# Kernel tuning notes

Hardware: AMD Instinct MI355X
Metric: run time of the kernel (lower is better)

The kernel has to match this reference:

```python
import jax, jax.numpy as jnp
import numpy as np

N_GAUSS = 1536
WIDTH, HEIGHT = 160, 128
FX = FY = 146.44        # 2343.024 * (160/2560)
CX, CY = WIDTH / 2.0, HEIGHT / 2.0
EPS2D = 0.3             # 2D covariance dilation (as in prepare_rasterization_coefficients)
NEAR, FAR = 0.01, 1e10


def eval_sh_basis(dirs):
    # real SH basis up to degree 3, 16 components (matches eval_sh_old)
    x, y, z = dirs[..., 0], dirs[..., 1], dirs[..., 2]
    one = jnp.ones_like(x)
    return jnp.stack([
        0.282095 * one,
        -0.488603 * y, 0.488603 * z, -0.488603 * x,
        1.092548 * x * y, -1.092548 * y * z, 0.315392 * (3 * z * z - 1),
        -1.092548 * x * z, 0.546274 * (x * x - y * y),
        -0.590044 * y * (3 * x * x - y * y), 2.890611 * x * y * z,
        -0.457046 * y * (5 * z * z - 1), 0.373176 * z * (5 * z * z - 3),
        -0.457046 * x * (5 * z * z - 1), 1.445306 * z * (x * x - y * y),
        -0.590044 * x * (x * x - 3 * y * y)], axis=-1)


def quat_to_rot(q):
    q = q / jnp.linalg.norm(q, axis=1, keepdims=True)
    w, x, y, z = q[:, 0], q[:, 1], q[:, 2], q[:, 3]
    R = jnp.stack([
        1 - 2 * (y * y + z * z), 2 * (x * y - z * w), 2 * (x * z + y * w),
        2 * (x * y + z * w), 1 - 2 * (x * x + z * z), 2 * (y * z - x * w),
        2 * (x * z - y * w), 2 * (y * z + x * w), 1 - 2 * (x * x + y * y)], axis=-1)
    return R.reshape(-1, 3, 3)


def get_viewmat(c2w):
    # c2w: (B,3,4); flip y/z camera axes then invert (matches torch get_viewmat)
    R = c2w[:, :3, :3] * jnp.array([[[1.0, -1.0, -1.0]]], dtype=c2w.dtype)
    t = c2w[:, :3, 3:4]
    R_inv = jnp.swapaxes(R, 1, 2)
    t_inv = -(R_inv @ t)
    return R_inv[0], t_inv[0, :, 0]


def setup_inputs() -> dict:
    key = jax.random.key(0)
    k0, k1, k2, k3, k4, k5 = jax.random.split(key, 6)
    N = N_GAUSS
    xy = jax.random.normal(k0, (N, 2), dtype=jnp.float32) * 0.5
    # world z negative -> positive camera-frame depth after axis flip
    z = -(1.0 + 4.0 * jax.random.uniform(k1, (N, 1), dtype=jnp.float32))
    means = jnp.concatenate([xy, z], axis=1)
    quats = jax.random.normal(k2, (N, 4), dtype=jnp.float32)
    log_scales = jax.random.normal(k3, (N, 3), dtype=jnp.float32) * 0.3 - 3.0
    opacity_logits = jax.random.normal(k4, (N,), dtype=jnp.float32)
    sh_coeffs = jax.random.normal(k5, (N, 16, 3), dtype=jnp.float32) * 0.3
    camera_to_worlds = jnp.eye(4, dtype=jnp.float32)[None, :3, :]
    return {"means": means, "quats": quats, "log_scales": log_scales,
            "opacity_logits": opacity_logits, "sh_coeffs": sh_coeffs,
            "camera_to_worlds": camera_to_worlds}


def reference(means, quats, log_scales, opacity_logits, sh_coeffs, camera_to_worlds):
    R_w2c, t_w2c = get_viewmat(camera_to_worlds)
    means_cam = means @ R_w2c.T + t_w2c                    # (N,3)
    depth = means_cam[:, 2]
    mask = (depth > NEAR) & (depth < FAR)

    # view-dependent colors from SH (degree 3)
    cam_pos = camera_to_worlds[0, :3, 3]
    dirs = means - cam_pos
    dirs = dirs / jnp.linalg.norm(dirs, axis=1, keepdims=True)
    colors = jnp.maximum(jnp.einsum('nk,nkc->nc', eval_sh_basis(dirs), sh_coeffs) + 0.5, 0.0)

    # 3D covariance -> camera frame -> EWA 2D projection
    Rg = quat_to_rot(quats)                                 # (N,3,3)
    M = Rg * jnp.exp(log_scales)[:, None, :]                # R @ diag(S)
    cov3d = M @ jnp.swapaxes(M, 1, 2)
    cov_cam = jnp.einsum('ij,njk,lk->nil', R_w2c, cov3d, R_w2c)
    tx, ty, tz = means_cam[:, 0], means_cam[:, 1], means_cam[:, 2]
    rz = 1.0 / tz
    zero = jnp.zeros_like(rz)
    J = jnp.stack([jnp.stack([FX * rz, zero, -FX * tx * rz * rz], -1),
                   jnp.stack([zero, FY * rz, -FY * ty * rz * rz], -1)], -2)  # (N,2,3)
    cov2d = jnp.einsum('nij,njk,nlk->nil', J, cov_cam, J)
    a = cov2d[:, 0, 0] + EPS2D
    c = cov2d[:, 1, 1] + EPS2D
    b = cov2d[:, 0, 1]
    det = a * c - b * b
    A, B, C = c / det, -b / det, a / det                    # conic (inverse 2D cov)

    u = FX * tx * rz + CX
    v = FY * ty * rz + CY
    opac = jax.nn.sigmoid(opacity_logits)

    px = jnp.arange(WIDTH, dtype=means.dtype)
    py = jnp.arange(HEIGHT, dtype=means.dtype)
    dx = px[None, None, :] - u[:, None, None]               # (N,1,W)
    dy = py[None, :, None] - v[:, None, None]               # (N,H,1)
    power = (-0.5 * (A[:, None, None] * dx * dx + C[:, None, None] * dy * dy)
             - B[:, None, None] * (dx * dy))                # (N,H,W)
    alpha = jnp.minimum(0.999, opac[:, None, None] * jnp.exp(power))
    alpha = jnp.where(mask[:, None, None], alpha, 0.0)

    # global depth sort (front-to-back alpha compositing)
    order = jnp.argsort(jnp.where(mask, depth, jnp.inf))
    alpha = alpha[order]
    colors = colors[order]
    T = jnp.cumprod(1.0 - alpha, axis=0)
    T_excl = jnp.concatenate([jnp.ones_like(T[:1]), T[:-1]], axis=0)
    w = T_excl * alpha                                      # (N,H,W)
    rgb = jnp.einsum('nhw,nc->hwc', w, colors)              # (H,W,3)
    return rgb
```

## Files before the change

### kernel.cpp

```cpp
#include <hip/hip_runtime.h>
#include <math.h>

#define N_GAUSS 1536
#define WIDTH   160
#define HEIGHT  128
#define NPIX    (WIDTH * HEIGHT)
#define FXC     146.44f
#define FYC     146.44f
#define CXC     80.0f
#define CYC     64.0f
#define EPS2D   0.3f
#define NEARP   0.01f
#define FARP    1e10f
#define CHUNK   128
#define NCHUNK  (N_GAUSS / CHUNK)
#define REC     12
#define L2E     1.4426950408889634f

#define PREP_BLOCKS 384
#define PREP_TPB    256
#define SCAN_LEN4   (N_GAUSS / 64 / 4)

__device__ __forceinline__ float fast_exp2(float x) {
    return __builtin_amdgcn_exp2f(x);
}


__global__ __launch_bounds__(PREP_TPB) void prep_sort_kernel(
    const float* __restrict__ means, const float* __restrict__ quats,
    const float* __restrict__ log_scales, const float* __restrict__ opac_logits,
    const float* __restrict__ sh, const float* __restrict__ c2w,
    float* __restrict__ sorted)
{
    __shared__ float4 k4_lds[N_GAUSS / 4];
    float* k_lds = (float*)k4_lds;

    float C[12];
#pragma unroll
    for (int k = 0; k < 12; k++) C[k] = c2w[k];
    float R00 =  C[0], R01 =  C[4], R02 =  C[8];
    float R10 = -C[1], R11 = -C[5], R12 = -C[9];
    float R20 = -C[2], R21 = -C[6], R22 = -C[10];
    float cpx = C[3], cpy = C[7], cpz = C[11];
    float t0 = -(R00 * cpx + R01 * cpy + R02 * cpz);
    float t1 = -(R10 * cpx + R11 * cpy + R12 * cpz);
    float t2 = -(R20 * cpx + R21 * cpy + R22 * cpz);

    for (int j = threadIdx.x; j < N_GAUSS; j += PREP_TPB) {
        float mx = means[3 * j], my = means[3 * j + 1], mz = means[3 * j + 2];
        float tzj = R20 * mx + R21 * my + R22 * mz + t2;
        bool m = (tzj > NEARP) && (tzj < FARP);
        k_lds[j] = m ? tzj : INFINITY;
    }
    __syncthreads();

    int i    = blockIdx.x * 4 + (threadIdx.x >> 6);
    int part = threadIdx.x & 63;

    float mx = means[3 * i], my = means[3 * i + 1], mz = means[3 * i + 2];
    float4 qv = ((const float4*)quats)[i];
    float lsx = log_scales[3 * i + 0];
    float lsy = log_scales[3 * i + 1];
    float lsz = log_scales[3 * i + 2];
    float olog = opac_logits[i];
    const float4* sh4 = (const float4*)(sh + i * 48);
    float4 S[12];
#pragma unroll
    for (int k = 0; k < 12; k++) S[k] = sh4[k];
    const float* shf = (const float*)S;

    float tx = R00 * mx + R01 * my + R02 * mz + t0;
    float ty = R10 * mx + R11 * my + R12 * mz + t1;
    float tz = R20 * mx + R21 * my + R22 * mz + t2;
    bool mask = (tz > NEARP) && (tz < FARP);

    float dx = mx - cpx, dy = my - cpy, dz = mz - cpz;
    float rn = rsqrtf(dx * dx + dy * dy + dz * dz);
    float x = dx * rn, y = dy * rn, z = dz * rn;
    float xx = x * x, yy = y * y, zz = z * z;
    float basis[16];
    basis[0]  = 0.282095f;
    basis[1]  = -0.488603f * y;
    basis[2]  = 0.488603f * z;
    basis[3]  = -0.488603f * x;
    basis[4]  = 1.092548f * x * y;
    basis[5]  = -1.092548f * y * z;
    basis[6]  = 0.315392f * (3.f * zz - 1.f);
    basis[7]  = -1.092548f * x * z;
    basis[8]  = 0.546274f * (xx - yy);
    basis[9]  = -0.590044f * y * (3.f * xx - yy);
    basis[10] = 2.890611f * x * y * z;
    basis[11] = -0.457046f * y * (5.f * zz - 1.f);
    basis[12] = 0.373176f * z * (5.f * zz - 3.f);
    basis[13] = -0.457046f * x * (5.f * zz - 1.f);
    basis[14] = 1.445306f * z * (xx - yy);
    basis[15] = -0.590044f * x * (xx - 3.f * yy);
    float cr = 0.f, cg = 0.f, cb = 0.f;
#pragma unroll
    for (int k = 0; k < 16; k++) {
        cr += basis[k] * shf[3 * k + 0];
        cg += basis[k] * shf[3 * k + 1];
        cb += basis[k] * shf[3 * k + 2];
    }
    cr = fmaxf(cr + 0.5f, 0.f);
    cg = fmaxf(cg + 0.5f, 0.f);
    cb = fmaxf(cb + 0.5f, 0.f);

    float qw = qv.x, qx = qv.y, qy = qv.z, qz = qv.w;
    float qn = rsqrtf(qw * qw + qx * qx + qy * qy + qz * qz);
    qw *= qn; qx *= qn; qy *= qn; qz *= qn;
    float sx = expf(lsx);
    float sy = expf(lsy);
    float sz = expf(lsz);
    float M00 = (1.f - 2.f * (qy * qy + qz * qz)) * sx;
    float M01 = (2.f * (qx * qy - qz * qw)) * sy;
    float M02 = (2.f * (qx * qz + qy * qw)) * sz;
    float M10 = (2.f * (qx * qy + qz * qw)) * sx;
    float M11 = (1.f - 2.f * (qx * qx + qz * qz)) * sy;
    float M12 = (2.f * (qy * qz - qx * qw)) * sz;
    float M20 = (2.f * (qx * qz - qy * qw)) * sx;
    float M21 = (2.f * (qy * qz + qx * qw)) * sy;
    float M22 = (1.f - 2.f * (qx * qx + qy * qy)) * sz;
    float V00 = M00 * M00 + M01 * M01 + M02 * M02;
    float V01 = M00 * M10 + M01 * M11 + M02 * M12;
    float V02 = M00 * M20 + M01 * M21 + M02 * M22;
    float V11 = M10 * M10 + M11 * M11 + M12 * M12;
    float V12 = M10 * M20 + M11 * M21 + M12 * M22;
    float V22 = M20 * M20 + M21 * M21 + M22 * M22;

    float T00 = R00 * V00 + R01 * V01 + R02 * V02;
    float T01 = R00 * V01 + R01 * V11 + R02 * V12;
    float T02 = R00 * V02 + R01 * V12 + R02 * V22;
    float T10 = R10 * V00 + R11 * V01 + R12 * V02;
    float T11 = R10 * V01 + R11 * V11 + R12 * V12;
    float T12 = R10 * V02 + R11 * V12 + R12 * V22;
    float T20 = R20 * V00 + R21 * V01 + R22 * V02;
    float T21 = R20 * V01 + R21 * V11 + R22 * V12;
    float T22 = R20 * V02 + R21 * V12 + R22 * V22;
    float cc00 = T00 * R00 + T01 * R01 + T02 * R02;
    float cc01 = T00 * R10 + T01 * R11 + T02 * R12;
    float cc02 = T00 * R20 + T01 * R21 + T02 * R22;
    float cc11 = T10 * R10 + T11 * R11 + T12 * R12;
    float cc12 = T10 * R20 + T11 * R21 + T12 * R22;
    float cc22 = T20 * R20 + T21 * R21 + T22 * R22;

    float rz = 1.f / tz;
    float rz2 = rz * rz;
    float j00 = FXC * rz, j02 = -FXC * tx * rz2;
    float j11 = FYC * rz, j12 = -FYC * ty * rz2;
    float c2d00 = j00 * j00 * cc00 + 2.f * j00 * j02 * cc02 + j02 * j02 * cc22;
    float c2d01 = (j00 * cc01 + j02 * cc12) * j11 + (j00 * cc02 + j02 * cc22) * j12;
    float c2d11 = j11 * j11 * cc11 + 2.f * j11 * j12 * cc12 + j12 * j12 * cc22;

    float a = c2d00 + EPS2D, c = c2d11 + EPS2D, b = c2d01;
    float idet = 1.f / (a * c - b * b);
    float Ac = c * idet, Bc = -b * idet, Cc = a * idet;
    float u = FXC * tx * rz + CXC;
    float v = FYC * ty * rz + CYC;
    float op = 1.f / (1.f + expf(-olog));
    float a2 = -0.5f * L2E * Ac;
    float b2 = -L2E * Bc;
    float c2 = -0.5f * L2E * Cc;
    float o2 = log2f(op);
    if (!mask) {
        u = 0.f; v = 0.f; a2 = 0.f; b2 = 0.f; c2 = 0.f; o2 = -INFINITY;
    }

    float ki = k_lds[i];
    int rank = 0;
    int base4 = part * SCAN_LEN4;
#pragma unroll
    for (int jj = 0; jj < SCAN_LEN4; jj++) {
        int j4 = base4 + jj;
        float4 kk = k4_lds[j4];
        int j = 4 * j4;
        rank += (kk.x < ki) || (kk.x == ki && (j + 0) < i);
        rank += (kk.y < ki) || (kk.y == ki && (j + 1) < i);
        rank += (kk.z < ki) || (kk.z == ki && (j + 2) < i);
        rank += (kk.w < ki) || (kk.w == ki && (j + 3) < i);
    }
    rank += __shfl_xor(rank, 1);
    rank += __shfl_xor(rank, 2);
    rank += __shfl_xor(rank, 4);
    rank += __shfl_xor(rank, 8);
    rank += __shfl_xor(rank, 16);
    rank += __shfl_xor(rank, 32);

    if (part == 0) {
        float4* dst = (float4*)(sorted + rank * REC);
        dst[0] = make_float4(u, v, a2, b2);
        dst[1] = make_float4(c2, o2, cr, cg);
        dst[2] = make_float4(cb, 0.f, 0.f, 0.f);
    }
}

__global__ __launch_bounds__(256) void raster_kernel(
    const float4* __restrict__ sorted4, float4* __restrict__ partial)
{
    const float4* src = sorted4 + blockIdx.y * (CHUNK * 3);

    int p = blockIdx.x * 256 + threadIdx.x;
    float px = (float)(p % WIDTH);
    float py = (float)(p / WIDTH);
    float T = 1.f, cr = 0.f, cg = 0.f, cb = 0.f;
#pragma unroll 4
    for (int j = 0; j < CHUNK; j++) {
        float4 f0 = src[3 * j + 0];
        float4 f1 = src[3 * j + 1];
        float4 f2 = src[3 * j + 2];
        float dx = px - f0.x;
        float dy = py - f0.y;
        float t  = f0.z * dx;
        t = fmaf(f0.w, dy, t);
        float q  = f1.x * dy;
        float pw = fmaf(t, dx, f1.y);
        pw = fmaf(q, dy, pw);
        float alpha = fminf(0.999f, fast_exp2(pw));
        float w = T * alpha;
        cr = fmaf(w, f1.z, cr);
        cg = fmaf(w, f1.w, cg);
        cb = fmaf(w, f2.x, cb);
        T -= w;
    }
    partial[blockIdx.y * NPIX + p] = make_float4(cr, cg, cb, T);
}

__global__ __launch_bounds__(256) void combine_kernel(
    const float4* __restrict__ partial, float4* __restrict__ out4)
{
    int t = blockIdx.x * 256 + threadIdx.x;
    int p = 4 * t;
    float T[4] = {1.f, 1.f, 1.f, 1.f};
    float r[4] = {0.f, 0.f, 0.f, 0.f};
    float g[4] = {0.f, 0.f, 0.f, 0.f};
    float b[4] = {0.f, 0.f, 0.f, 0.f};
#pragma unroll
    for (int c = 0; c < NCHUNK; c++) {
        const float4* row = partial + c * NPIX + p;
#pragma unroll
        for (int k = 0; k < 4; k++) {
            float4 q = row[k];
            r[k] = fmaf(T[k], q.x, r[k]);
            g[k] = fmaf(T[k], q.y, g[k]);
            b[k] = fmaf(T[k], q.z, b[k]);
            T[k] *= q.w;
        }
    }
    out4[3 * t + 0] = make_float4(r[0], g[0], b[0], r[1]);
    out4[3 * t + 1] = make_float4(g[1], b[1], r[2], g[2]);
    out4[3 * t + 2] = make_float4(b[2], r[3], g[3], b[3]);
}

extern "C" void kernel_launch(void* const* d_in, const int* in_sizes, int n_in,
                              void* d_out, int out_size, void* d_ws, size_t ws_size,
                              hipStream_t stream) {
    const float* means       = (const float*)d_in[0];
    const float* quats       = (const float*)d_in[1];
    const float* log_scales  = (const float*)d_in[2];
    const float* opac_logits = (const float*)d_in[3];
    const float* sh          = (const float*)d_in[4];
    const float* c2w         = (const float*)d_in[5];

    float* ws     = (float*)d_ws;
    float* sorted = ws;
    float4* partial = (float4*)(sorted + N_GAUSS * REC);

    prep_sort_kernel<<<PREP_BLOCKS, PREP_TPB, 0, stream>>>(
        means, quats, log_scales, opac_logits, sh, c2w, sorted);
    raster_kernel<<<dim3(NPIX / 256, NCHUNK), 256, 0, stream>>>(
        (const float4*)sorted, partial);
    combine_kernel<<<NPIX / 1024, 256, 0, stream>>>(partial, (float4*)d_out);
}
```

Before: 90.37 us.

## Fuse chunked rasterization and compositing combine into one kernel via LDS

```diff
diff --git a/kernel.cpp b/kernel.cpp
--- a/kernel.cpp
+++ b/kernel.cpp
@@ -12,14 +12,16 @@
 #define EPS2D   0.3f
 #define NEARP   0.01f
 #define FARP    1e10f
-#define CHUNK   128
-#define NCHUNK  (N_GAUSS / CHUNK)
 #define REC     12
 #define L2E     1.4426950408889634f
 
 #define PREP_BLOCKS 384
 #define PREP_TPB    256
 #define SCAN_LEN4   (N_GAUSS / 64 / 4)
+
+#define NWAVE   16
+#define RCHUNK  (N_GAUSS / NWAVE)
+#define RPIX    64
 
 __device__ __forceinline__ float fast_exp2(float x) {
     return __builtin_amdgcn_exp2f(x);
@@ -194,17 +196,22 @@
     }
 }
 
-__global__ __launch_bounds__(256) void raster_kernel(
-    const float4* __restrict__ sorted4, float4* __restrict__ partial)
+__global__ __launch_bounds__(1024) void raster_kernel(
+    const float4* __restrict__ sorted4, float* __restrict__ out)
 {
-    const float4* src = sorted4 + blockIdx.y * (CHUNK * 3);
-
-    int p = blockIdx.x * 256 + threadIdx.x;
+    __shared__ float4 part_lds[NWAVE * RPIX];
+
+    int wave = threadIdx.x >> 6;
+    int lane = threadIdx.x & 63;
+    int p = blockIdx.x * RPIX + lane;
     float px = (float)(p % WIDTH);
     float py = (float)(p / WIDTH);
+
+    const float4* src = sorted4 + wave * (RCHUNK * 3);
+
     float T = 1.f, cr = 0.f, cg = 0.f, cb = 0.f;
 #pragma unroll 4
-    for (int j = 0; j < CHUNK; j++) {
+    for (int j = 0; j < RCHUNK; j++) {
         float4 f0 = src[3 * j + 0];
         float4 f1 = src[3 * j + 1];
         float4 f2 = src[3 * j + 2];
@@ -222,33 +229,24 @@
         cb = fmaf(w, f2.x, cb);
         T -= w;
     }
-    partial[blockIdx.y * NPIX + p] = make_float4(cr, cg, cb, T);
-}
-
-__global__ __launch_bounds__(256) void combine_kernel(
-    const float4* __restrict__ partial, float4* __restrict__ out4)
-{
-    int t = blockIdx.x * 256 + threadIdx.x;
-    int p = 4 * t;
-    float T[4] = {1.f, 1.f, 1.f, 1.f};
-    float r[4] = {0.f, 0.f, 0.f, 0.f};
-    float g[4] = {0.f, 0.f, 0.f, 0.f};
-    float b[4] = {0.f, 0.f, 0.f, 0.f};
-#pragma unroll
-    for (int c = 0; c < NCHUNK; c++) {
-        const float4* row = partial + c * NPIX + p;
-#pragma unroll
-        for (int k = 0; k < 4; k++) {
-            float4 q = row[k];
-            r[k] = fmaf(T[k], q.x, r[k]);
-            g[k] = fmaf(T[k], q.y, g[k]);
-            b[k] = fmaf(T[k], q.z, b[k]);
-            T[k] *= q.w;
+    part_lds[wave * RPIX + lane] = make_float4(cr, cg, cb, T);
+    __syncthreads();
+
+    if (threadIdx.x < RPIX) {
+        int pp = blockIdx.x * RPIX + threadIdx.x;
+        float Tt = 1.f, r = 0.f, g = 0.f, b = 0.f;
+#pragma unroll
+        for (int c = 0; c < NWAVE; c++) {
+            float4 q = part_lds[c * RPIX + threadIdx.x];
+            r = fmaf(Tt, q.x, r);
+            g = fmaf(Tt, q.y, g);
+            b = fmaf(Tt, q.z, b);
+            Tt *= q.w;
         }
-    }
-    out4[3 * t + 0] = make_float4(r[0], g[0], b[0], r[1]);
-    out4[3 * t + 1] = make_float4(g[1], b[1], r[2], g[2]);
-    out4[3 * t + 2] = make_float4(b[2], r[3], g[3], b[3]);
+        out[3 * pp + 0] = r;
+        out[3 * pp + 1] = g;
+        out[3 * pp + 2] = b;
+    }
 }
 
 extern "C" void kernel_launch(void* const* d_in, const int* in_sizes, int n_in,
@@ -263,11 +261,9 @@
 
     float* ws     = (float*)d_ws;
     float* sorted = ws;
-    float4* partial = (float4*)(sorted + N_GAUSS * REC);
 
     prep_sort_kernel<<<PREP_BLOCKS, PREP_TPB, 0, stream>>>(
         means, quats, log_scales, opac_logits, sh, c2w, sorted);
-    raster_kernel<<<dim3(NPIX / 256, NCHUNK), 256, 0, stream>>>(
-        (const float4*)sorted, partial);
-    combine_kernel<<<NPIX / 1024, 256, 0, stream>>>(partial, (float4*)d_out);
-}
+    raster_kernel<<<NPIX / RPIX, NWAVE * 64, 0, stream>>>(
+        (const float4*)sorted, (float*)d_out);
+}
```

Measured after the change: 118.0 us. 30.6% more time.
